# Kernel tuning notes

Measured on AMD Instinct MI355X. Metric: run time of the kernel, lower is better.

Reference implementation:

```python
import jax, jax.numpy as jnp
import numpy as np

NEG_INF = -1.0e7


def positional_encodings(max_seq_len, hidden_size):
    pos = jnp.arange(max_seq_len, dtype=jnp.float32)[:, None]
    dim = jnp.arange(hidden_size // 2, dtype=jnp.float32)[None, :]
    args = pos / (10000.0 ** (2.0 * dim / hidden_size))  # (max_seq_len, h/2)
    pe = jnp.zeros((max_seq_len, hidden_size), dtype=jnp.float32)
    pe = pe.at[:, 0::2].set(jnp.sin(args)).at[:, 1::2].set(jnp.cos(args))
    return pe


def _attention(x_q, x_kv, Wq, bq, Wk, bk, Wv, bv, scale, causal):
    # Linear layers (torch Linear: y = x @ W^T + b; here W stored as (in, out)).
    q = x_q @ Wq + bq            # (B, Sq, H)
    k = x_kv @ Wk + bk           # (B, Sk, H)
    v = x_kv @ Wv + bv           # (B, Sk, H)
    scores = jnp.einsum('bqh,bkh->bqk', q, k) * scale  # (B, Sq, Sk)
    if causal:
        sq, sk = scores.shape[1], scores.shape[2]
        # original adds neg_inf * tril(ones, diag=-1) on (B, Sk, Sq): masked when k_idx > q_idx
        mask = (jnp.arange(sk)[None, :] > jnp.arange(sq)[:, None]).astype(scores.dtype)
        scores = scores + NEG_INF * mask
    w = jax.nn.softmax(scores, axis=-1)                # (B, Sq, Sk)
    ctx = jnp.einsum('bqk,bkh->bqh', w, v)
    return ctx, jnp.transpose(w, (0, 2, 1))            # weights returned as (B, Sk, Sq)


def setup_inputs() -> dict:
    B, S_dec, S_enc, H, V, L = 8, 512, 512, 1024, 32000, 6
    key = jax.random.key(0)
    ks = jax.random.split(key, 20)
    s = 0.02
    inp = {
        'inputs': jax.random.randint(ks[0], (B, S_dec), 0, V),
        'annotations': jax.random.normal(ks[1], (B, S_enc, H), dtype=jnp.float32),
        'hidden_init': jnp.zeros((B, H), dtype=jnp.float32),
        'embedding': jax.random.normal(ks[2], (V, H), dtype=jnp.float32) * s,
        'Wq_s': jax.random.normal(ks[3], (L, H, H), dtype=jnp.float32) * s,
        'bq_s': jnp.zeros((L, H), dtype=jnp.float32),
        'Wk_s': jax.random.normal(ks[4], (L, H, H), dtype=jnp.float32) * s,
        'bk_s': jnp.zeros((L, H), dtype=jnp.float32),
        'Wv_s': jax.random.normal(ks[5], (L, H, H), dtype=jnp.float32) * s,
        'bv_s': jnp.zeros((L, H), dtype=jnp.float32),
        'Wq_c': jax.random.normal(ks[6], (L, H, H), dtype=jnp.float32) * s,
        'bq_c': jnp.zeros((L, H), dtype=jnp.float32),
        'Wk_c': jax.random.normal(ks[7], (L, H, H), dtype=jnp.float32) * s,
        'bk_c': jnp.zeros((L, H), dtype=jnp.float32),
        'Wv_c': jax.random.normal(ks[8], (L, H, H), dtype=jnp.float32) * s,
        'bv_c': jnp.zeros((L, H), dtype=jnp.float32),
        'Wm': jax.random.normal(ks[9], (L, H, H), dtype=jnp.float32) * s,
        'bm': jnp.zeros((L, H), dtype=jnp.float32),
        'Wout': jax.random.normal(ks[10], (H, V), dtype=jnp.float32) * s,
        'bout': jnp.zeros((V,), dtype=jnp.float32),
    }
    return inp


def reference(inputs, annotations, hidden_init, embedding,
              Wq_s, bq_s, Wk_s, bk_s, Wv_s, bv_s,
              Wq_c, bq_c, Wk_c, bk_c, Wv_c, bv_c,
              Wm, bm, Wout, bout):
    B, S = inputs.shape
    L, H, _ = Wq_s.shape
    scale = 1.0 / jnp.sqrt(jnp.asarray(H, dtype=jnp.float32))
    pe = positional_encodings(1000, H)
    contexts = embedding[inputs] + pe[:S]              # (B, S, H)
    enc_ws, self_ws = [], []
    for i in range(L):
        new_ctx, sw = _attention(contexts, contexts,
                                 Wq_s[i], bq_s[i], Wk_s[i], bk_s[i], Wv_s[i], bv_s[i],
                                 scale, causal=True)
        residual = contexts + new_ctx
        new_ctx, ew = _attention(residual, annotations,
                                 Wq_c[i], bq_c[i], Wk_c[i], bk_c[i], Wv_c[i], bv_c[i],
                                 scale, causal=False)
        residual = residual + new_ctx
        mlp = jax.nn.relu(residual @ Wm[i] + bm[i])
        contexts = residual + mlp
        enc_ws.append(ew)
        self_ws.append(sw)
    output = contexts @ Wout + bout                    # (B, S, V)
    return output, (jnp.stack(enc_ws), jnp.stack(self_ws))
```

## Files before the change

### kernel.cpp

```cpp
#include <hip/hip_runtime.h>

typedef __attribute__((ext_vector_type(4))) float f4;
typedef __attribute__((ext_vector_type(8))) short s8v;
typedef __attribute__((ext_vector_type(4))) short s4v;

__device__ __forceinline__ short f2bf(float f) {
  union { float f; unsigned int u; } v; v.f = f;
  unsigned int u = v.u;
  unsigned int r = 0x7fffu + ((u >> 16) & 1u);
  return (short)((u + r) >> 16);
}

__device__ __forceinline__ void glds16(const void* g, void* l) {
  __builtin_amdgcn_global_load_lds((const __attribute__((address_space(1))) void*)g,
                                   (__attribute__((address_space(3))) void*)l, 16, 0, 0);
}

template<int BIAS, int RES, int RELU, int OF32, int OBF, int VT>
__global__ __launch_bounds__(256) void gemmp(
    const unsigned short* __restrict__ A, const unsigned short* __restrict__ Bt,
    const float* __restrict__ bias, const float* __restrict__ bias2,
    const float* __restrict__ res,
    float* __restrict__ Cf, unsigned short* __restrict__ Cb,
    unsigned short* __restrict__ Cvt, int vtoff, int ldvt,
    int lda, int ldb, int ldc, int ldcb, int ldr, int nk,
    long sA, long sB, long sC, long sCb, long sR, long sBias, long sVt) {
  __shared__ __align__(1024) char lds[98304];
  int tid = threadIdx.x;
  int bx = blockIdx.x, by = blockIdx.y, bz = blockIdx.z;
  int bm0 = by * 128, bn0 = bx * 128;
  const char* Ag = (const char*)(A + bz * sA);
  const char* Bg = (const char*)(Bt + bz * sB);
  if (BIAS) bias += bz * sBias;
  int w = tid >> 6, lane = tid & 63;
  int sr = tid >> 3;
  int skb = ((tid & 7) ^ (sr & 7)) << 4;
  size_t la2 = (size_t)lda * 2, lb2 = (size_t)ldb * 2;
  char* bf0 = lds;
  char* bf1 = lds + 32768;
  char* bf2 = lds + 65536;
  int wm = (w >> 1) * 64, wn = (w & 1) * 64;
  int rb = lane & 15;
  int kx = (lane & 7) << 4;
  int kb0 = (lane >> 4) << 4;
  f4 acc[4][4] = {};

  auto stageH = [&](char* buf, int kt, int h) {
    size_t ka = (size_t)kt * 128 + skb;
    if (h == 0) {
      glds16(Ag + (size_t)(bm0 + sr) * la2 + ka,            buf + w * 1024);
      glds16(Ag + (size_t)(bm0 + 32 + sr) * la2 + ka,       buf + 4096 + w * 1024);
      glds16(Bg + (size_t)(bn0 + sr) * lb2 + ka,            buf + 16384 + w * 1024);
      glds16(Bg + (size_t)(bn0 + 32 + sr) * lb2 + ka,       buf + 20480 + w * 1024);
    } else {
      glds16(Ag + (size_t)(bm0 + 64 + sr) * la2 + ka,       buf + 8192 + w * 1024);
      glds16(Ag + (size_t)(bm0 + 96 + sr) * la2 + ka,       buf + 12288 + w * 1024);
      glds16(Bg + (size_t)(bn0 + 64 + sr) * lb2 + ka,       buf + 24576 + w * 1024);
      glds16(Bg + (size_t)(bn0 + 96 + sr) * lb2 + ka,       buf + 28672 + w * 1024);
    }
  };
  auto phase = [&](const char* buf, int ks) {
    const char* Ar = buf + (wm + rb) * 128;
    const char* Br = buf + 16384 + (wn + rb) * 128;
    int kb = (kb0 + ks * 64) ^ kx;
    s8v a[4], b[4];
#pragma unroll
    for (int i = 0; i < 4; ++i) a[i] = *(const s8v*)(Ar + i * 2048 + kb);
#pragma unroll
    for (int j = 0; j < 4; ++j) b[j] = *(const s8v*)(Br + j * 2048 + kb);
    __builtin_amdgcn_s_setprio(1);
#pragma unroll
    for (int i = 0; i < 4; ++i)
#pragma unroll
      for (int j = 0; j < 4; ++j)
        acc[i][j] = __builtin_amdgcn_mfma_f32_16x16x32_bf16(b[j], a[i], acc[i][j], 0, 0, 0);
    __builtin_amdgcn_s_setprio(0);
  };

  stageH(bf0, 0, 0); stageH(bf0, 0, 1);
  stageH(bf1, 1, 0); stageH(bf1, 1, 1);

  for (int t = 0; t < nk - 2; ++t) {
    stageH(bf2, t + 2, 0);
    asm volatile("s_waitcnt vmcnt(12)" ::: "memory");
    __builtin_amdgcn_s_barrier();
    __builtin_amdgcn_sched_barrier(0);
    phase(bf0, 0);
    __builtin_amdgcn_s_barrier();
    stageH(bf2, t + 2, 1);
    __builtin_amdgcn_s_barrier();
    __builtin_amdgcn_sched_barrier(0);
    phase(bf0, 1);
    __builtin_amdgcn_s_barrier();
    char* tp = bf0; bf0 = bf1; bf1 = bf2; bf2 = tp;
  }
  asm volatile("s_waitcnt vmcnt(8)" ::: "memory");
  __builtin_amdgcn_s_barrier();
  __builtin_amdgcn_sched_barrier(0);
  phase(bf0, 0);
  __builtin_amdgcn_s_barrier();
  __builtin_amdgcn_sched_barrier(0);
  phase(bf0, 1);
  __builtin_amdgcn_s_barrier();
  asm volatile("s_waitcnt vmcnt(0)" ::: "memory");
  __builtin_amdgcn_s_barrier();
  __builtin_amdgcn_sched_barrier(0);
  phase(bf1, 0);
  phase(bf1, 1);

  __syncthreads();
  if (VT && bn0 >= vtoff) {
    float* Et = (float*)lds;
#pragma unroll
    for (int i = 0; i < 4; ++i) {
      int lr = wm + i * 16 + (lane & 15);
#pragma unroll
      for (int j = 0; j < 4; ++j) {
        int col0 = wn + j * 16 + ((lane >> 4) << 2);
#pragma unroll
        for (int c = 0; c < 4; ++c) Et[(col0 + c) * 132 + lr] = acc[i][j][c];
      }
    }
    __syncthreads();
    unsigned short* Vp = Cvt + bz * sVt;
    int hb = bn0 - vtoff;
#pragma unroll
    for (int p = 0; p < 16; ++p) {
      int fi = p * 256 + tid;
      int h = fi >> 5, m4 = (fi & 31) * 4;
      f4 v = *(const f4*)&Et[h * 132 + m4];
      float bb = (BIAS == 1) ? bias[bn0 + h] : 0.f;
      s4v o;
      o[0] = f2bf(v[0] + bb); o[1] = f2bf(v[1] + bb);
      o[2] = f2bf(v[2] + bb); o[3] = f2bf(v[3] + bb);
      *(s4v*)(Vp + (size_t)(hb + h) * ldvt + bm0 + m4) = o;
    }
  } else {
    float* E = (float*)lds;
#pragma unroll
    for (int i = 0; i < 4; ++i) {
      int lr = wm + i * 16 + (lane & 15);
      int sw = (lr & 7) << 2;
#pragma unroll
      for (int j = 0; j < 4; ++j) {
        int col = wn + j * 16 + ((lane >> 4) << 2);
        *(f4*)&E[lr * 128 + (col ^ sw)] = acc[i][j];
      }
    }
    __syncthreads();
    float* Cfp = Cf + bz * sC;
    unsigned short* Cbp = Cb + bz * sCb;
    const float* Rp = res + bz * sR;
#pragma unroll
    for (int p = 0; p < 16; ++p) {
      int fi = p * 256 + tid;
      int row = fi >> 5, c4 = fi & 31;
      f4 v = *(const f4*)&E[row * 128 + ((c4 ^ (row & 7)) << 2)];
      int rr = bm0 + row;
      int col = bn0 + c4 * 4;
      if (BIAS == 1) { v[0] += bias[col]; v[1] += bias[col+1]; v[2] += bias[col+2]; v[3] += bias[col+3]; }
      if (BIAS == 2) { float bb = bias[rr]; v[0] += bb; v[1] += bb; v[2] += bb; v[3] += bb; }
      if (RELU) { v[0]=fmaxf(v[0],0.f); v[1]=fmaxf(v[1],0.f); v[2]=fmaxf(v[2],0.f); v[3]=fmaxf(v[3],0.f); }
      if (RES) { f4 rv = *(const f4*)(Rp + (size_t)rr * ldr + col); v[0]+=rv[0]; v[1]+=rv[1]; v[2]+=rv[2]; v[3]+=rv[3]; }
      if (OF32) *(f4*)(Cfp + (size_t)rr * ldc + col) = v;
      if (OBF) {
        s4v o; o[0]=f2bf(v[0]); o[1]=f2bf(v[1]); o[2]=f2bf(v[2]); o[3]=f2bf(v[3]);
        *(s4v*)(Cbp + (size_t)rr * ldcb + col) = o;
      }
    }
  }
}

template<int RES, int OF32, int OBF>
__global__ __launch_bounds__(256) void gemm64(
    const unsigned short* __restrict__ A, const unsigned short* __restrict__ Bt,
    const float* __restrict__ res,
    float* __restrict__ Cf, unsigned short* __restrict__ Cb,
    int lda, int ldb, int ldc, int ldcb, int ldr, int nk,
    long sA, long sB, long sC, long sCb, long sR) {
  __shared__ __align__(16) char smem[16384];
  int tid = threadIdx.x;
  int bx = blockIdx.x, by = blockIdx.y, bz = blockIdx.z;
  int bm0 = by * 64, bn0 = bx * 64;
  const char* Ag = (const char*)(A + bz * sA);
  const char* Bg = (const char*)(Bt + bz * sB);
  int w = tid >> 6, lane = tid & 63;
  int sr = tid >> 3;
  int skb = ((tid & 7) ^ (sr & 7)) << 4;
  size_t la2 = (size_t)lda * 2, lb2 = (size_t)ldb * 2;
  char* Al = smem + w * 1024;
  char* Bl = smem + 8192 + w * 1024;
  int wm = (w >> 1) * 32, wn = (w & 1) * 32;
  int rb = lane & 15;
  int kx = (lane & 7) << 4;
  int kb0 = (lane >> 4) << 4;
  const char* Ar = smem + (wm + rb) * 128;
  const char* Br = smem + 8192 + (wn + rb) * 128;
  f4 acc[2][2] = {};
  for (int kt = 0; kt < nk; ++kt) {
    size_t ka = (size_t)kt * 128 + skb;
    __syncthreads();
#pragma unroll
    for (int p = 0; p < 2; ++p)
      glds16(Ag + (size_t)(bm0 + p * 32 + sr) * la2 + ka, Al + p * 4096);
#pragma unroll
    for (int p = 0; p < 2; ++p)
      glds16(Bg + (size_t)(bn0 + p * 32 + sr) * lb2 + ka, Bl + p * 4096);
    __syncthreads();
#pragma unroll
    for (int ks = 0; ks < 2; ++ks) {
      int kb = (kb0 + ks * 64) ^ kx;
      s8v a[2], b[2];
#pragma unroll
      for (int i = 0; i < 2; ++i) a[i] = *(const s8v*)(Ar + i * 2048 + kb);
#pragma unroll
      for (int j = 0; j < 2; ++j) b[j] = *(const s8v*)(Br + j * 2048 + kb);
#pragma unroll
      for (int i = 0; i < 2; ++i)
#pragma unroll
        for (int j = 0; j < 2; ++j)
          acc[i][j] = __builtin_amdgcn_mfma_f32_16x16x32_bf16(b[j], a[i], acc[i][j], 0, 0, 0);
    }
  }
  float* Cfp = Cf + bz * sC;
  unsigned short* Cbp = Cb + bz * sCb;
  const float* Rp = res + bz * sR;
  float* E = (float*)smem;
  __syncthreads();
#pragma unroll
  for (int i = 0; i < 2; ++i) {
    int lr = wm + i * 16 + (lane & 15);
    int sw = (lr & 7) << 2;
#pragma unroll
    for (int j = 0; j < 2; ++j) {
      int col = wn + j * 16 + ((lane >> 4) << 2);
      *(f4*)&E[lr * 64 + (col ^ sw)] = acc[i][j];
    }
  }
  __syncthreads();
#pragma unroll
  for (int p = 0; p < 4; ++p) {
    int fi = p * 256 + tid;
    int row = fi >> 4, c4 = fi & 15;
    f4 v = *(const f4*)&E[row * 64 + ((c4 ^ (row & 7)) << 2)];
    int rr = bm0 + row;
    int col = bn0 + c4 * 4;
    if (RES) { f4 rv = *(const f4*)(Rp + (size_t)rr * ldr + col); v[0]+=rv[0]; v[1]+=rv[1]; v[2]+=rv[2]; v[3]+=rv[3]; }
    if (OF32) *(f4*)(Cfp + (size_t)rr * ldc + col) = v;
    if (OBF) {
      s4v o; o[0]=f2bf(v[0]); o[1]=f2bf(v[1]); o[2]=f2bf(v[2]); o[3]=f2bf(v[3]);
      *(s4v*)(Cbp + (size_t)rr * ldcb + col) = o;
    }
  }
}

__global__ __launch_bounds__(512) void gemm_logits(
    const unsigned short* __restrict__ A, const unsigned short* __restrict__ Bt,
    const float* __restrict__ bias, float* __restrict__ C) {
  __shared__ __align__(1024) char lds[147456];
  const int ldc = 32000, nk = 16;
  int tid = threadIdx.x;
  int w = tid >> 6, lane = tid & 63;
  int id = blockIdx.y * 250 + blockIdx.x;
  int k = id & 7, j = id >> 3;
  int by = ((k >> 1) << 2) + (j & 3);
  int bx = (k & 1) * 125 + (j >> 2);
  int bm0 = by * 256, bn0 = bx * 128;
  const size_t ld2 = 2048;
  const char* Ag = (const char*)A;
  const char* Bg = (const char*)Bt;
  int srow = (w << 3) + (lane >> 3);
  size_t ska = (size_t)(((lane & 7) ^ (lane >> 3)) << 4);
  char* bf0 = lds;
  char* bf1 = lds + 49152;
  char* bf2 = lds + 98304;
  int wm = (w >> 1) * 64;
  int wn = (w & 1) * 64;
  int rsel = lane & 15;
  int kx = (lane & 7) << 4;
  int kb0 = (lane >> 4) << 4;
  f4 acc[4][4] = {};

  auto stageH = [&](char* buf, int kt, int h) {
    size_t ka = (size_t)kt * 128 + ska;
    if (h == 0) {
      glds16(Ag + (size_t)(bm0 + srow) * ld2 + ka,       buf + w * 1024);
      glds16(Ag + (size_t)(bm0 + 64 + srow) * ld2 + ka,  buf + 8192 + w * 1024);
      glds16(Bg + (size_t)(bn0 + srow) * ld2 + ka,       buf + 32768 + w * 1024);
    } else {
      glds16(Ag + (size_t)(bm0 + 128 + srow) * ld2 + ka, buf + 16384 + w * 1024);
      glds16(Ag + (size_t)(bm0 + 192 + srow) * ld2 + ka, buf + 24576 + w * 1024);
      glds16(Bg + (size_t)(bn0 + 64 + srow) * ld2 + ka,  buf + 40960 + w * 1024);
    }
  };
  auto phase = [&](const char* buf, int ks) {
    const char* Ab = buf + (wm + rsel) * 128;
    const char* Bb = buf + 32768 + (wn + rsel) * 128;
    int kb = (kb0 + ks * 64) ^ kx;
    s8v a0 = *(const s8v*)(Ab + kb);
    s8v a1 = *(const s8v*)(Ab + 2048 + kb);
    s8v a2 = *(const s8v*)(Ab + 4096 + kb);
    s8v a3 = *(const s8v*)(Ab + 6144 + kb);
    s8v q0 = *(const s8v*)(Bb + kb);
    s8v q1 = *(const s8v*)(Bb + 2048 + kb);
    s8v q2 = *(const s8v*)(Bb + 4096 + kb);
    s8v q3 = *(const s8v*)(Bb + 6144 + kb);
    __builtin_amdgcn_s_setprio(1);
    acc[0][0] = __builtin_amdgcn_mfma_f32_16x16x32_bf16(q0, a0, acc[0][0], 0, 0, 0);
    acc[0][1] = __builtin_amdgcn_mfma_f32_16x16x32_bf16(q1, a0, acc[0][1], 0, 0, 0);
    acc[0][2] = __builtin_amdgcn_mfma_f32_16x16x32_bf16(q2, a0, acc[0][2], 0, 0, 0);
    acc[0][3] = __builtin_amdgcn_mfma_f32_16x16x32_bf16(q3, a0, acc[0][3], 0, 0, 0);
    acc[1][0] = __builtin_amdgcn_mfma_f32_16x16x32_bf16(q0, a1, acc[1][0], 0, 0, 0);
    acc[1][1] = __builtin_amdgcn_mfma_f32_16x16x32_bf16(q1, a1, acc[1][1], 0, 0, 0);
    acc[1][2] = __builtin_amdgcn_mfma_f32_16x16x32_bf16(q2, a1, acc[1][2], 0, 0, 0);
    acc[1][3] = __builtin_amdgcn_mfma_f32_16x16x32_bf16(q3, a1, acc[1][3], 0, 0, 0);
    acc[2][0] = __builtin_amdgcn_mfma_f32_16x16x32_bf16(q0, a2, acc[2][0], 0, 0, 0);
    acc[2][1] = __builtin_amdgcn_mfma_f32_16x16x32_bf16(q1, a2, acc[2][1], 0, 0, 0);
    acc[2][2] = __builtin_amdgcn_mfma_f32_16x16x32_bf16(q2, a2, acc[2][2], 0, 0, 0);
    acc[2][3] = __builtin_amdgcn_mfma_f32_16x16x32_bf16(q3, a2, acc[2][3], 0, 0, 0);
    acc[3][0] = __builtin_amdgcn_mfma_f32_16x16x32_bf16(q0, a3, acc[3][0], 0, 0, 0);
    acc[3][1] = __builtin_amdgcn_mfma_f32_16x16x32_bf16(q1, a3, acc[3][1], 0, 0, 0);
    acc[3][2] = __builtin_amdgcn_mfma_f32_16x16x32_bf16(q2, a3, acc[3][2], 0, 0, 0);
    acc[3][3] = __builtin_amdgcn_mfma_f32_16x16x32_bf16(q3, a3, acc[3][3], 0, 0, 0);
    __builtin_amdgcn_s_setprio(0);
  };

  stageH(bf0, 0, 0); stageH(bf0, 0, 1);
  stageH(bf1, 1, 0); stageH(bf1, 1, 1);

  for (int t = 0; t < nk - 2; ++t) {
    stageH(bf2, t + 2, 0);
    asm volatile("s_waitcnt vmcnt(9)" ::: "memory");
    __builtin_amdgcn_s_barrier();
    __builtin_amdgcn_sched_barrier(0);
    phase(bf0, 0);
    __builtin_amdgcn_s_barrier();
    stageH(bf2, t + 2, 1);
    __builtin_amdgcn_s_barrier();
    __builtin_amdgcn_sched_barrier(0);
    phase(bf0, 1);
    __builtin_amdgcn_s_barrier();
    char* tp = bf0; bf0 = bf1; bf1 = bf2; bf2 = tp;
  }
  asm volatile("s_waitcnt vmcnt(6)" ::: "memory");
  __builtin_amdgcn_s_barrier();
  __builtin_amdgcn_sched_barrier(0);
  phase(bf0, 0);
  __builtin_amdgcn_s_barrier();
  __builtin_amdgcn_sched_barrier(0);
  phase(bf0, 1);
  __builtin_amdgcn_s_barrier();
  asm volatile("s_waitcnt vmcnt(0)" ::: "memory");
  __builtin_amdgcn_s_barrier();
  __builtin_amdgcn_sched_barrier(0);
  phase(bf1, 0);
  phase(bf1, 1);

  float* E = (float*)lds;
  __syncthreads();
#pragma unroll
  for (int i = 0; i < 4; ++i) {
    int lr = wm + i * 16 + (lane & 15);
    int sw = (lr & 7) << 2;
#pragma unroll
    for (int j = 0; j < 4; ++j) {
      int col = wn + j * 16 + ((lane >> 4) << 2);
      *(f4*)&E[lr * 128 + (col ^ sw)] = acc[i][j];
    }
  }
  __syncthreads();
#pragma unroll
  for (int p = 0; p < 16; ++p) {
    int fi = p * 512 + tid;
    int row = fi >> 5, c4 = fi & 31;
    f4 v = *(const f4*)&E[row * 128 + ((c4 ^ (row & 7)) << 2)];
    int rr = bm0 + row;
    int col = bn0 + c4 * 4;
    v[0] += bias[col]; v[1] += bias[col+1]; v[2] += bias[col+2]; v[3] += bias[col+3];
    __builtin_nontemporal_store(v, (f4*)(C + (size_t)rr * ldc + col));
  }
}

__device__ __forceinline__ void wtrans_tile(const float* src, unsigned short* dst,
                                            int rows, int cols, int c0, int r0) {
  __shared__ float t[64][65];
  int tx = threadIdx.x & 63, ty = threadIdx.x >> 6;
#pragma unroll
  for (int j = 0; j < 16; ++j) {
    int r = j * 4 + ty;
    t[r][tx] = src[(size_t)(r0 + r) * cols + c0 + tx];
  }
  __syncthreads();
#pragma unroll
  for (int j = 0; j < 16; ++j) {
    int n = j * 4 + ty;
    dst[(size_t)(c0 + n) * rows + r0 + tx] = (unsigned short)f2bf(t[tx][n]);
  }
}

__global__ __launch_bounds__(256) void wtrans_k(const float* __restrict__ src,
                                                unsigned short* __restrict__ dst,
                                                int rows, int cols) {
  wtrans_tile(src, dst, rows, cols, blockIdx.x * 64, blockIdx.y * 64);
}

__global__ __launch_bounds__(256) void wtrans_all_k(
    const float* __restrict__ w0, const float* __restrict__ w1,
    const float* __restrict__ w2, const float* __restrict__ w3,
    const float* __restrict__ w4, const float* __restrict__ w5,
    const float* __restrict__ w6, unsigned short* __restrict__ dst) {
  int z = blockIdx.z;
  int l = z / 7, wi = z % 7;
  const float* src;
  switch (wi) {
    case 0: src = w0; break;
    case 1: src = w1; break;
    case 2: src = w2; break;
    case 3: src = w3; break;
    case 4: src = w4; break;
    case 5: src = w5; break;
    default: src = w6; break;
  }
  src += (size_t)l * 1024 * 1024;
  unsigned short* d = dst + (size_t)z * 1024 * 1024;
  wtrans_tile(src, d, 1024, 1024, blockIdx.x * 64, blockIdx.y * 64);
}

__global__ __launch_bounds__(256) void convbf_k(const float* __restrict__ src,
                                                unsigned short* __restrict__ dst, int n4) {
  int i = blockIdx.x * 256 + threadIdx.x;
  if (i >= n4) return;
  f4 f = ((const f4*)src)[i];
  s4v v;
  v[0] = f2bf(f[0]); v[1] = f2bf(f[1]); v[2] = f2bf(f[2]); v[3] = f2bf(f[3]);
  ((s4v*)dst)[i] = v;
}

__global__ __launch_bounds__(1024) void catb_k(
    const float* __restrict__ bq, const float* __restrict__ bk,
    const float* __restrict__ bv, const float* __restrict__ bkc,
    const float* __restrict__ bvc, float* __restrict__ catb,
    float* __restrict__ catbc) {
  int l = blockIdx.x, t = threadIdx.x;
  size_t o = (size_t)l * 1024 + t;
  catb[(size_t)l * 3072 + t] = bq[o];
  catb[(size_t)l * 3072 + 1024 + t] = bk[o];
  catb[(size_t)l * 3072 + 2048 + t] = bv[o];
  catbc[(size_t)l * 2048 + t] = bkc[o];
  catbc[(size_t)l * 2048 + 1024 + t] = bvc[o];
}

template<int CAUSAL>
__global__ __launch_bounds__(512) void smt_k(const float* __restrict__ Sf,
                                             float* __restrict__ outT,
                                             unsigned short* __restrict__ Wb) {
  __shared__ float T[32][524];
  int b = blockIdx.y;
  int q0 = blockIdx.x * 32;
  int t = threadIdx.x;
  const float* Sp = Sf + ((size_t)b * 512 + q0) * 512;
#pragma unroll
  for (int j = 0; j < 8; ++j) {
    int idx = t + 512 * j;
    int r = idx >> 7, c4 = idx & 127;
    f4 v = *(const f4*)(Sp + (size_t)r * 512 + c4 * 4);
    *(f4*)&T[r][c4 * 4] = v;
  }
  __syncthreads();
  int w = t >> 6, l = t & 63;
  int r = 4 * w + (l >> 4);
  int l16 = l & 15;
  int q = q0 + r;
  const float scale = 0.03125f;
  float v[32];
#pragma unroll
  for (int j = 0; j < 32; ++j) {
    int k = l16 + 16 * j;
    float x = T[r][k] * scale;
    if (CAUSAL && k > q) x += -1.0e7f;
    v[j] = x;
  }
  float m = v[0];
#pragma unroll
  for (int j = 1; j < 32; ++j) m = fmaxf(m, v[j]);
  m = fmaxf(m, __shfl_xor(m, 1)); m = fmaxf(m, __shfl_xor(m, 2));
  m = fmaxf(m, __shfl_xor(m, 4)); m = fmaxf(m, __shfl_xor(m, 8));
  float s = 0.f;
#pragma unroll
  for (int j = 0; j < 32; ++j) { v[j] = __expf(v[j] - m); s += v[j]; }
  s += __shfl_xor(s, 1); s += __shfl_xor(s, 2);
  s += __shfl_xor(s, 4); s += __shfl_xor(s, 8);
  float inv = 1.0f / s;
#pragma unroll
  for (int j = 0; j < 32; ++j) T[r][l16 + 16 * j] = v[j] * inv;
  __syncthreads();
  float* op = outT + (size_t)b * 512 * 512 + q0;
  int ql = t & 31, kb = t >> 5;
#pragma unroll
  for (int i = 0; i < 32; ++i) {
    int k = kb + 16 * i;
    __builtin_nontemporal_store(T[ql][k], &op[(size_t)k * 512 + ql]);
  }
  unsigned short* wp = Wb + ((size_t)b * 512 + q0) * 512;
#pragma unroll
  for (int i = 0; i < 4; ++i) {
    int rr = 4 * w + i;
    const float* row = &T[rr][l * 8];
    s8v o;
#pragma unroll
    for (int j = 0; j < 8; ++j) o[j] = f2bf(row[j]);
    *(s8v*)(wp + (size_t)rr * 512 + l * 8) = o;
  }
}

__global__ __launch_bounds__(256) void embed_pe_k(const int* __restrict__ ids,
                                                  const float* __restrict__ emb,
                                                  float* __restrict__ ctx,
                                                  unsigned short* __restrict__ ctxb) {
  int row = blockIdx.x;
  int s = row & 511;
  int t = threadIdx.x;
  int id = ids[row];
  f4 e = *(const f4*)(emb + (size_t)id * 1024 + t * 4);
  int j0 = 2 * t, j1 = 2 * t + 1;
  float fr0 = powf(10000.0f, -2.0f * (float)j0 / 1024.0f);
  float fr1 = powf(10000.0f, -2.0f * (float)j1 / 1024.0f);
  float s0, c0, s1, c1;
  sincosf((float)s * fr0, &s0, &c0);
  sincosf((float)s * fr1, &s1, &c1);
  f4 o;
  o[0] = e[0] + s0; o[1] = e[1] + c0; o[2] = e[2] + s1; o[3] = e[3] + c1;
  *(f4*)(ctx + (size_t)row * 1024 + t * 4) = o;
  s4v ob;
  ob[0] = f2bf(o[0]); ob[1] = f2bf(o[1]); ob[2] = f2bf(o[2]); ob[3] = f2bf(o[3]);
  *(s4v*)(ctxb + (size_t)row * 1024 + t * 4) = ob;
}

extern "C" void kernel_launch(void* const* d_in, const int* in_sizes, int n_in,
                              void* d_out, int out_size, void* d_ws, size_t ws_size,
                              hipStream_t stream) {
  const int B = 8, S = 512, H = 1024, V = 32000, L = 6;
  const int M = B * S;

  const int* ids = (const int*)d_in[0];
  const float* ann = (const float*)d_in[1];
  const float* emb = (const float*)d_in[3];
  const float* bq_s = (const float*)d_in[5];
  const float* bk_s = (const float*)d_in[7];
  const float* bv_s = (const float*)d_in[9];
  const float* bq_c = (const float*)d_in[11];
  const float* bk_c = (const float*)d_in[13];
  const float* bv_c = (const float*)d_in[15];
  const float* bm = (const float*)d_in[17];
  const float* Wout = (const float*)d_in[18];
  const float* bout = (const float*)d_in[19];
  float* out = (float*)d_out;

  char* ws = (char*)d_ws;
  if (ws_size < ((size_t)164 << 20)) return;
  float* X0 = (float*)ws;
  unsigned short* Xs0 = (unsigned short*)(ws + ((size_t)16 << 20));
  unsigned short* Xs1 = (unsigned short*)(ws + ((size_t)24 << 20));
  unsigned short* QKbf = (unsigned short*)(ws + ((size_t)32 << 20));
  unsigned short* Vtbf = (unsigned short*)(ws + ((size_t)48 << 20));
  float* Sbuf = (float*)(ws + ((size_t)56 << 20));
  unsigned short* Wbf = (unsigned short*)(ws + ((size_t)64 << 20));
  unsigned short* annbf = (unsigned short*)(ws + ((size_t)68 << 20));
  unsigned short* WT = (unsigned short*)(ws + ((size_t)76 << 20));
  float* catb = (float*)(ws + ((size_t)160 << 20));
  float* catbc = (float*)(ws + ((size_t)160 << 20) + (96 << 10));
  unsigned short* KcAll = (unsigned short*)d_out;
  unsigned short* VtcAll = (unsigned short*)((char*)d_out + ((size_t)48 << 20));

  size_t enc_off = (size_t)M * V;
  size_t self_off = enc_off + (size_t)L * B * S * S;

  long sQ = (long)S * H;
  long sS = (long)S * S;
  const size_t WSZ = (size_t)H * H;
  const long sW7 = (long)(7 * WSZ);

  embed_pe_k<<<M, 256, 0, stream>>>(ids, emb, X0, Xs0);
  convbf_k<<<(M * H / 4 + 255) / 256, 256, 0, stream>>>(ann, annbf, M * H / 4);
  catb_k<<<L, 1024, 0, stream>>>(bq_s, bk_s, bv_s, bk_c, bv_c, catb, catbc);
  wtrans_all_k<<<dim3(16, 16, 42), 256, 0, stream>>>(
      (const float*)d_in[4], (const float*)d_in[6], (const float*)d_in[8],
      (const float*)d_in[10], (const float*)d_in[12], (const float*)d_in[14],
      (const float*)d_in[16], WT);
  gemmp<1, 0, 0, 0, 1, 1><<<dim3(16, 32, 6), 256, 0, stream>>>(
      annbf, WT + 4 * WSZ, catbc, nullptr, nullptr,
      nullptr, KcAll, VtcAll, 1024, M,
      H, H, 0, H, 0, 16,
      0, sW7, 0, (long)M * H, 0, 2048, (long)H * M);

  unsigned short* Xa = Xs0;
  unsigned short* Xb = Xs1;

  for (int l = 0; l < L; ++l) {
    size_t bo = (size_t)l * H;
    unsigned short* WTl = WT + (size_t)l * 7 * WSZ;

    gemmp<1, 0, 0, 0, 1, 1><<<dim3(24, 32), 256, 0, stream>>>(
        Xa, WTl, catb + (size_t)l * 3072, nullptr, nullptr,
        nullptr, QKbf, Vtbf, 2048, M,
        H, H, 0, 2048, 0, 16,
        0, 0, 0, 0, 0, 0, 0);
    gemm64<0, 1, 0><<<dim3(8, 8, B), 256, 0, stream>>>(
        QKbf, QKbf + 1024, nullptr, Sbuf, nullptr,
        2048, 2048, S, 0, 0, 16, (long)S * 2048, (long)S * 2048, sS, 0, 0);
    smt_k<1><<<dim3(16, B), 512, 0, stream>>>(
        Sbuf, out + self_off + (size_t)l * B * S * S, Wbf);
    gemm64<1, 1, 1><<<dim3(16, 8, B), 256, 0, stream>>>(
        Wbf, Vtbf, X0, X0, Xb,
        S, M, H, H, H, 8, sS, 512, sQ, sQ, sQ);
    gemmp<1, 0, 0, 0, 1, 0><<<dim3(8, 32), 256, 0, stream>>>(
        Xb, WTl + 3 * WSZ, bq_c + bo, nullptr, nullptr,
        nullptr, QKbf, nullptr, 0, 0,
        H, H, 0, 1024, 0, 16,
        0, 0, 0, 0, 0, 0, 0);
    gemm64<0, 1, 0><<<dim3(8, 8, B), 256, 0, stream>>>(
        QKbf, KcAll + (size_t)l * M * H, nullptr, Sbuf, nullptr,
        1024, 1024, S, 0, 0, 16, (long)S * 1024, (long)S * 1024, sS, 0, 0);
    smt_k<0><<<dim3(16, B), 512, 0, stream>>>(
        Sbuf, out + enc_off + (size_t)l * B * S * S, Wbf);
    gemm64<1, 1, 1><<<dim3(16, 8, B), 256, 0, stream>>>(
        Wbf, VtcAll + (size_t)l * H * M, X0, X0, Xa,
        S, M, H, H, H, 8, sS, 512, sQ, sQ, sQ);
    gemmp<1, 1, 1, 1, 1, 0><<<dim3(8, 32), 256, 0, stream>>>(
        Xa, WTl + 6 * WSZ, bm + bo, nullptr, X0,
        X0, Xb, nullptr, 0, 0,
        H, H, H, H, H, 16,
        0, 0, 0, 0, 0, 0, 0);
    unsigned short* tb = Xa; Xa = Xb; Xb = tb;
  }

  wtrans_k<<<dim3(V / 64, H / 64), 256, 0, stream>>>(Wout, WT, H, V);
  gemm_logits<<<dim3(250, 16), 512, 0, stream>>>(Xa, WT, bout, out);
}
```

Measured before the change: 1.433 ms.

## Double-buffer gemm64 loads and shrink logits GEMM tile to 256x64

The gemm64 kernel moves from a single-buffer load-sync-compute loop to a double-buffered LDS pipeline, so the next K-tile's global-to-LDS loads overlap the current MFMA work, and it raises MFMA priority. The logits GEMM goes from 256x128 tiles with triple buffering to 256x64 tiles with double buffering and 80KB of LDS. That doubles the grid and may allow more blocks per CU, at the cost of lower per-block data reuse and more re-reads of the A matrix.

```diff
diff --git a/kernel.cpp b/kernel.cpp
--- a/kernel.cpp
+++ b/kernel.cpp
@@ -178,7 +178,7 @@
     float* __restrict__ Cf, unsigned short* __restrict__ Cb,
     int lda, int ldb, int ldc, int ldcb, int ldr, int nk,
     long sA, long sB, long sC, long sCb, long sR) {
-  __shared__ __align__(16) char smem[16384];
+  __shared__ __align__(1024) char smem[32768];
   int tid = threadIdx.x;
   int bx = blockIdx.x, by = blockIdx.y, bz = blockIdx.z;
   int bm0 = by * 64, bn0 = bx * 64;
@@ -188,25 +188,24 @@
   int sr = tid >> 3;
   int skb = ((tid & 7) ^ (sr & 7)) << 4;
   size_t la2 = (size_t)lda * 2, lb2 = (size_t)ldb * 2;
-  char* Al = smem + w * 1024;
-  char* Bl = smem + 8192 + w * 1024;
+  char* b0 = smem;
+  char* b1 = smem + 16384;
   int wm = (w >> 1) * 32, wn = (w & 1) * 32;
   int rb = lane & 15;
   int kx = (lane & 7) << 4;
   int kb0 = (lane >> 4) << 4;
-  const char* Ar = smem + (wm + rb) * 128;
-  const char* Br = smem + 8192 + (wn + rb) * 128;
   f4 acc[2][2] = {};
-  for (int kt = 0; kt < nk; ++kt) {
+
+  auto stage = [&](char* buf, int kt) {
     size_t ka = (size_t)kt * 128 + skb;
-    __syncthreads();
-#pragma unroll
-    for (int p = 0; p < 2; ++p)
-      glds16(Ag + (size_t)(bm0 + p * 32 + sr) * la2 + ka, Al + p * 4096);
-#pragma unroll
-    for (int p = 0; p < 2; ++p)
-      glds16(Bg + (size_t)(bn0 + p * 32 + sr) * lb2 + ka, Bl + p * 4096);
-    __syncthreads();
+    glds16(Ag + (size_t)(bm0 + sr) * la2 + ka,      buf + w * 1024);
+    glds16(Ag + (size_t)(bm0 + 32 + sr) * la2 + ka, buf + 4096 + w * 1024);
+    glds16(Bg + (size_t)(bn0 + sr) * lb2 + ka,      buf + 8192 + w * 1024);
+    glds16(Bg + (size_t)(bn0 + 32 + sr) * lb2 + ka, buf + 12288 + w * 1024);
+  };
+  auto compute = [&](const char* buf) {
+    const char* Ar = buf + (wm + rb) * 128;
+    const char* Br = buf + 8192 + (wn + rb) * 128;
 #pragma unroll
     for (int ks = 0; ks < 2; ++ks) {
       int kb = (kb0 + ks * 64) ^ kx;
@@ -215,13 +214,31 @@
       for (int i = 0; i < 2; ++i) a[i] = *(const s8v*)(Ar + i * 2048 + kb);
 #pragma unroll
       for (int j = 0; j < 2; ++j) b[j] = *(const s8v*)(Br + j * 2048 + kb);
+      __builtin_amdgcn_s_setprio(1);
 #pragma unroll
       for (int i = 0; i < 2; ++i)
 #pragma unroll
         for (int j = 0; j < 2; ++j)
           acc[i][j] = __builtin_amdgcn_mfma_f32_16x16x32_bf16(b[j], a[i], acc[i][j], 0, 0, 0);
-    }
-  }
+      __builtin_amdgcn_s_setprio(0);
+    }
+  };
+
+  stage(b0, 0);
+  for (int t = 0; t < nk - 1; ++t) {
+    stage(b1, t + 1);
+    asm volatile("s_waitcnt vmcnt(4)" ::: "memory");
+    __builtin_amdgcn_s_barrier();
+    __builtin_amdgcn_sched_barrier(0);
+    compute(b0);
+    __builtin_amdgcn_s_barrier();
+    char* tp = b0; b0 = b1; b1 = tp;
+  }
+  asm volatile("s_waitcnt vmcnt(0)" ::: "memory");
+  __builtin_amdgcn_s_barrier();
+  __builtin_amdgcn_sched_barrier(0);
+  compute(b0);
+
   float* Cfp = Cf + bz * sC;
   unsigned short* Cbp = Cb + bz * sCb;
   const float* Rp = res + bz * sR;
@@ -257,41 +274,36 @@
 __global__ __launch_bounds__(512) void gemm_logits(
     const unsigned short* __restrict__ A, const unsigned short* __restrict__ Bt,
     const float* __restrict__ bias, float* __restrict__ C) {
-  __shared__ __align__(1024) char lds[147456];
+  __shared__ __align__(1024) char lds[81920];
   const int ldc = 32000, nk = 16;
   int tid = threadIdx.x;
   int w = tid >> 6, lane = tid & 63;
-  int id = blockIdx.y * 250 + blockIdx.x;
+  int id = blockIdx.y * 500 + blockIdx.x;
   int k = id & 7, j = id >> 3;
   int by = ((k >> 1) << 2) + (j & 3);
-  int bx = (k & 1) * 125 + (j >> 2);
-  int bm0 = by * 256, bn0 = bx * 128;
+  int bx = (k & 1) * 250 + (j >> 2);
+  int bm0 = by * 256, bn0 = bx * 64;
   const size_t ld2 = 2048;
   const char* Ag = (const char*)A;
   const char* Bg = (const char*)Bt;
   int srow = (w << 3) + (lane >> 3);
   size_t ska = (size_t)(((lane & 7) ^ (lane >> 3)) << 4);
   char* bf0 = lds;
-  char* bf1 = lds + 49152;
-  char* bf2 = lds + 98304;
+  char* bf1 = lds + 40960;
   int wm = (w >> 1) * 64;
-  int wn = (w & 1) * 64;
+  int wn = (w & 1) * 32;
   int rsel = lane & 15;
   int kx = (lane & 7) << 4;
   int kb0 = (lane >> 4) << 4;
-  f4 acc[4][4] = {};
-
-  auto stageH = [&](char* buf, int kt, int h) {
+  f4 acc[4][2] = {};
+
+  auto stage = [&](char* buf, int kt) {
     size_t ka = (size_t)kt * 128 + ska;
-    if (h == 0) {
-      glds16(Ag + (size_t)(bm0 + srow) * ld2 + ka,       buf + w * 1024);
-      glds16(Ag + (size_t)(bm0 + 64 + srow) * ld2 + ka,  buf + 8192 + w * 1024);
-      glds16(Bg + (size_t)(bn0 + srow) * ld2 + ka,       buf + 32768 + w * 1024);
-    } else {
-      glds16(Ag + (size_t)(bm0 + 128 + srow) * ld2 + ka, buf + 16384 + w * 1024);
-      glds16(Ag + (size_t)(bm0 + 192 + srow) * ld2 + ka, buf + 24576 + w * 1024);
-      glds16(Bg + (size_t)(bn0 + 64 + srow) * ld2 + ka,  buf + 40960 + w * 1024);
-    }
+    glds16(Ag + (size_t)(bm0 + srow) * ld2 + ka,       buf + w * 1024);
+    glds16(Ag + (size_t)(bm0 + 64 + srow) * ld2 + ka,  buf + 8192 + w * 1024);
+    glds16(Ag + (size_t)(bm0 + 128 + srow) * ld2 + ka, buf + 16384 + w * 1024);
+    glds16(Ag + (size_t)(bm0 + 192 + srow) * ld2 + ka, buf + 24576 + w * 1024);
+    glds16(Bg + (size_t)(bn0 + srow) * ld2 + ka,       buf + 32768 + w * 1024);
   };
   auto phase = [&](const char* buf, int ks) {
     const char* Ab = buf + (wm + rsel) * 128;
@@ -303,77 +315,53 @@
     s8v a3 = *(const s8v*)(Ab + 6144 + kb);
     s8v q0 = *(const s8v*)(Bb + kb);
     s8v q1 = *(const s8v*)(Bb + 2048 + kb);
-    s8v q2 = *(const s8v*)(Bb + 4096 + kb);
-    s8v q3 = *(const s8v*)(Bb + 6144 + kb);
     __builtin_amdgcn_s_setprio(1);
     acc[0][0] = __builtin_amdgcn_mfma_f32_16x16x32_bf16(q0, a0, acc[0][0], 0, 0, 0);
     acc[0][1] = __builtin_amdgcn_mfma_f32_16x16x32_bf16(q1, a0, acc[0][1], 0, 0, 0);
-    acc[0][2] = __builtin_amdgcn_mfma_f32_16x16x32_bf16(q2, a0, acc[0][2], 0, 0, 0);
-    acc[0][3] = __builtin_amdgcn_mfma_f32_16x16x32_bf16(q3, a0, acc[0][3], 0, 0, 0);
     acc[1][0] = __builtin_amdgcn_mfma_f32_16x16x32_bf16(q0, a1, acc[1][0], 0, 0, 0);
     acc[1][1] = __builtin_amdgcn_mfma_f32_16x16x32_bf16(q1, a1, acc[1][1], 0, 0, 0);
-    acc[1][2] = __builtin_amdgcn_mfma_f32_16x16x32_bf16(q2, a1, acc[1][2], 0, 0, 0);
-    acc[1][3] = __builtin_amdgcn_mfma_f32_16x16x32_bf16(q3, a1, acc[1][3], 0, 0, 0);
     acc[2][0] = __builtin_amdgcn_mfma_f32_16x16x32_bf16(q0, a2, acc[2][0], 0, 0, 0);
     acc[2][1] = __builtin_amdgcn_mfma_f32_16x16x32_bf16(q1, a2, acc[2][1], 0, 0, 0);
-    acc[2][2] = __builtin_amdgcn_mfma_f32_16x16x32_bf16(q2, a2, acc[2][2], 0, 0, 0);
-    acc[2][3] = __builtin_amdgcn_mfma_f32_16x16x32_bf16(q3, a2, acc[2][3], 0, 0, 0);
     acc[3][0] = __builtin_amdgcn_mfma_f32_16x16x32_bf16(q0, a3, acc[3][0], 0, 0, 0);
     acc[3][1] = __builtin_amdgcn_mfma_f32_16x16x32_bf16(q1, a3, acc[3][1], 0, 0, 0);
-    acc[3][2] = __builtin_amdgcn_mfma_f32_16x16x32_bf16(q2, a3, acc[3][2], 0, 0, 0);
-    acc[3][3] = __builtin_amdgcn_mfma_f32_16x16x32_bf16(q3, a3, acc[3][3], 0, 0, 0);
     __builtin_amdgcn_s_setprio(0);
   };
 
-  stageH(bf0, 0, 0); stageH(bf0, 0, 1);
-  stageH(bf1, 1, 0); stageH(bf1, 1, 1);
-
-  for (int t = 0; t < nk - 2; ++t) {
-    stageH(bf2, t + 2, 0);
-    asm volatile("s_waitcnt vmcnt(9)" ::: "memory");
+  stage(bf0, 0);
+  for (int t = 0; t < nk - 1; ++t) {
+    stage(bf1, t + 1);
+    asm volatile("s_waitcnt vmcnt(5)" ::: "memory");
     __builtin_amdgcn_s_barrier();
     __builtin_amdgcn_sched_barrier(0);
     phase(bf0, 0);
-    __builtin_amdgcn_s_barrier();
-    stageH(bf2, t + 2, 1);
-    __builtin_amdgcn_s_barrier();
-    __builtin_amdgcn_sched_barrier(0);
     phase(bf0, 1);
     __builtin_amdgcn_s_barrier();
-    char* tp = bf0; bf0 = bf1; bf1 = bf2; bf2 = tp;
-  }
-  asm volatile("s_waitcnt vmcnt(6)" ::: "memory");
+    char* tp = bf0; bf0 = bf1; bf1 = tp;
+  }
+  asm volatile("s_waitcnt vmcnt(0)" ::: "memory");
   __builtin_amdgcn_s_barrier();
   __builtin_amdgcn_sched_barrier(0);
   phase(bf0, 0);
-  __builtin_amdgcn_s_barrier();
-  __builtin_amdgcn_sched_barrier(0);
   phase(bf0, 1);
-  __builtin_amdgcn_s_barrier();
-  asm volatile("s_waitcnt vmcnt(0)" ::: "memory");
-  __builtin_amdgcn_s_barrier();
-  __builtin_amdgcn_sched_barrier(0);
-  phase(bf1, 0);
-  phase(bf1, 1);
 
   float* E = (float*)lds;
   __syncthreads();
 #pragma unroll
   for (int i = 0; i < 4; ++i) {
-    int lr = wm + i * 16 + (lane & 15);
+    int lr = wm + i * 16 + rsel;
     int sw = (lr & 7) << 2;
 #pragma unroll
-    for (int j = 0; j < 4; ++j) {
+    for (int j = 0; j < 2; ++j) {
       int col = wn + j * 16 + ((lane >> 4) << 2);
-      *(f4*)&E[lr * 128 + (col ^ sw)] = acc[i][j];
-    }
-  }
-  __syncthreads();
-#pragma unroll
-  for (int p = 0; p < 16; ++p) {
+      *(f4*)&E[lr * 64 + (col ^ sw)] = acc[i][j];
+    }
+  }
+  __syncthreads();
+#pragma unroll
+  for (int p = 0; p < 8; ++p) {
     int fi = p * 512 + tid;
-    int row = fi >> 5, c4 = fi & 31;
-    f4 v = *(const f4*)&E[row * 128 + ((c4 ^ (row & 7)) << 2)];
+    int row = fi >> 4, c4 = fi & 15;
+    f4 v = *(const f4*)&E[row * 64 + ((c4 ^ (row & 7)) << 2)];
     int rr = bm0 + row;
     int col = bn0 + c4 * 4;
     v[0] += bias[col]; v[1] += bias[col+1]; v[2] += bias[col+2]; v[3] += bias[col+3];
@@ -635,5 +623,5 @@
   }
 
   wtrans_k<<<dim3(V / 64, H / 64), 256, 0, stream>>>(Wout, WT, H, V);
-  gemm_logits<<<dim3(250, 16), 512, 0, stream>>>(Xa, WT, bout, out);
-}
+  gemm_logits<<<dim3(500, 16), 512, 0, stream>>>(Xa, WT, bout, out);
+}
```

After: 1.396 ms. 1.03x faster.
